# Performance work log

Measured on AMD Instinct MI355X. Metric: run time of the kernel, lower is better.

## Reference

```python
import jax, jax.numpy as jnp
import numpy as np

D_MODEL = 1024
N_HEADS = 16
D_K = D_MODEL // N_HEADS  # 64, also d_v
B, S = 8, 1024


def setup_inputs() -> dict:
    key = jax.random.key(0)
    ks = jax.random.split(key, 12)
    sc = 1.0 / np.sqrt(D_MODEL)
    inp = {
        "q": jax.random.normal(ks[0], (B, S, D_MODEL), jnp.float32),
        "k": jax.random.normal(ks[1], (B, S, D_MODEL), jnp.float32),
        "v": jax.random.normal(ks[2], (B, S, D_MODEL), jnp.float32),
        # per-head projection weights stacked over heads; torch Linear stores [out,in]
        "Wq": jax.random.normal(ks[3], (N_HEADS, D_K, D_MODEL), jnp.float32) * sc,
        "bq": jax.random.normal(ks[4], (N_HEADS, D_K), jnp.float32) * sc,
        "Wk": jax.random.normal(ks[5], (N_HEADS, D_K, D_MODEL), jnp.float32) * sc,
        "bk": jax.random.normal(ks[6], (N_HEADS, D_K), jnp.float32) * sc,
        "Wv": jax.random.normal(ks[7], (N_HEADS, D_K, D_MODEL), jnp.float32) * sc,
        "bv": jax.random.normal(ks[8], (N_HEADS, D_K), jnp.float32) * sc,
        "Wf": jax.random.normal(ks[9], (D_MODEL, D_MODEL), jnp.float32) * sc,
        "bf": jax.random.normal(ks[10], (D_MODEL,), jnp.float32) * sc,
    }
    return inp


def reference(q, k, v, Wq, bq, Wk, bk, Wv, bv, Wf, bf):
    temper = jnp.asarray(D_K ** 0.5, q.dtype)
    # per-head linear projections, all heads at once: [b,s,h,dk]
    qh = jnp.einsum('bsd,hkd->bhsk', q, Wq) + bq[None, :, None, :]
    kh = jnp.einsum('bsd,hkd->bhsk', k, Wk) + bk[None, :, None, :]
    vh = jnp.einsum('bsd,hkd->bhsk', v, Wv) + bv[None, :, None, :]
    # scaled dot-product scores [b,h,s,s]
    scores = jnp.einsum('bhik,bhjk->bhij', qh, kh) / temper
    # faithful scalar-equality mask: positions exactly equal to mask (=0) -> -inf
    scores = jnp.where(scores == 0.0, -jnp.inf, scores)
    attn = jax.nn.softmax(scores, axis=-1)
    out = jnp.einsum('bhij,bhjv->bhiv', attn, vh)  # [b,h,s,dv]
    # concat heads (head order matches torch.cat over ModuleList)
    out = out.transpose(0, 2, 1, 3).reshape(out.shape[0], out.shape[2], -1)  # [b,s,d_model]
    return out @ Wf.T + bf
```

## Files before the change

### kernel.cpp

```cpp
#include <hip/hip_runtime.h>
#include <hip/hip_bf16.h>


#define D_MODEL_ 1024
#define NH_ 16
#define DK_ 64
#define B_ 8
#define S_ 1024
#define M_ (B_ * S_)

typedef __hip_bfloat16 bf16;
typedef __attribute__((ext_vector_type(8))) short short8;
typedef __attribute__((ext_vector_type(4))) short short4_t;
typedef __attribute__((ext_vector_type(4))) float f32x4;

typedef const __attribute__((address_space(1))) unsigned int* gas_u32p;
typedef __attribute__((address_space(3))) unsigned int* las_u32p;

__device__ __forceinline__ short f2bs(float x) {
  bf16 h = __float2bfloat16(x);
  return *reinterpret_cast<short*>(&h);
}

__global__ __launch_bounds__(256)
void conv_f32_bf16(const float* __restrict__ in, bf16* __restrict__ out) {
  size_t i = ((size_t)blockIdx.x * 256 + threadIdx.x) * 8;
  f32x4 a = *(const f32x4*)(in + i);
  f32x4 b = *(const f32x4*)(in + i + 4);
  short8 s;
  s[0] = f2bs(a[0]); s[1] = f2bs(a[1]); s[2] = f2bs(a[2]); s[3] = f2bs(a[3]);
  s[4] = f2bs(b[0]); s[5] = f2bs(b[1]); s[6] = f2bs(b[2]); s[7] = f2bs(b[3]);
  *(short8*)((short*)out + i) = s;
}

__global__ __launch_bounds__(256)
void conv_w4(const float* __restrict__ w0, const float* __restrict__ w1,
             const float* __restrict__ w2, const float* __restrict__ w3,
             bf16* __restrict__ out) {
  const float* src = (blockIdx.z == 0) ? w0 : (blockIdx.z == 1) ? w1
                   : (blockIdx.z == 2) ? w2 : w3;
  size_t i = ((size_t)blockIdx.x * 256 + threadIdx.x) * 8;
  f32x4 a = *(const f32x4*)(src + i);
  f32x4 b = *(const f32x4*)(src + i + 4);
  short8 s;
  s[0] = f2bs(a[0]); s[1] = f2bs(a[1]); s[2] = f2bs(a[2]); s[3] = f2bs(a[3]);
  s[4] = f2bs(b[0]); s[5] = f2bs(b[1]); s[6] = f2bs(b[2]); s[7] = f2bs(b[3]);
  *(short8*)((short*)out + (size_t)blockIdx.z * 1024 * 1024 + i) = s;
}

__global__ __launch_bounds__(256)
void gemm_mfma(const void* __restrict__ A, const bf16* __restrict__ Wb,
               const float* __restrict__ bias, void* __restrict__ C,
               int aF32, int cMode, float cscale)
{
  __shared__ short As[2][2][128 * 32];
  __shared__ short Bs[2][2][128 * 32];
  const int tid = threadIdx.x;
  const int lane = tid & 63;
  const int w = tid >> 6;
  const int l15 = lane & 15, quad = lane >> 4;
  const int wm = (w >> 1) * 64, wn = (w & 1) * 64;
  const int m0 = blockIdx.x * 128, n0 = blockIdx.y * 128;

  const int srow = (lane >> 2);
  const int skc  = (lane & 3) * 8;

  f32x4 au[4], av[4];

  auto stageA = [&](int buf, int k0) {
    const bf16* Ab = (const bf16*)A;
#pragma unroll
    for (int sub = 0; sub < 2; ++sub)
#pragma unroll
      for (int p = 0; p < 2; ++p) {
        int r = 32 * w + 16 * p + srow;
        __builtin_amdgcn_global_load_lds(
            (gas_u32p)(const void*)(Ab + (size_t)(m0 + r) * 1024 + k0 + sub * 32 + skc),
            (las_u32p)(void*)((char*)&As[buf][sub][0] + w * 2048 + p * 1024), 16, 0, 0);
      }
  };
  auto stageB = [&](int buf, int k0) {
#pragma unroll
    for (int sub = 0; sub < 2; ++sub)
#pragma unroll
      for (int p = 0; p < 2; ++p) {
        int r = 32 * w + 16 * p + srow;
        __builtin_amdgcn_global_load_lds(
            (gas_u32p)(const void*)(Wb + (size_t)(n0 + r) * 1024 + k0 + sub * 32 + skc),
            (las_u32p)(void*)((char*)&Bs[buf][sub][0] + w * 2048 + p * 1024), 16, 0, 0);
      }
  };
  auto loadAf = [&](int k0) {
    const float* Af = (const float*)A;
#pragma unroll
    for (int p = 0; p < 4; ++p) {
      int c = p * 256 + tid;
      int r = c >> 3, kc = (c & 7) * 8;
      const float* g = Af + (size_t)(m0 + r) * 1024 + k0 + kc;
      au[p] = *(const f32x4*)g;
      av[p] = *(const f32x4*)(g + 4);
    }
  };
  auto writeAf = [&](int buf) {
#pragma unroll
    for (int p = 0; p < 4; ++p) {
      int c = p * 256 + tid;
      int r = c >> 3, kc = (c & 7) * 8;
      short8 s;
      s[0] = f2bs(au[p][0]); s[1] = f2bs(au[p][1]); s[2] = f2bs(au[p][2]); s[3] = f2bs(au[p][3]);
      s[4] = f2bs(av[p][0]); s[5] = f2bs(av[p][1]); s[6] = f2bs(av[p][2]); s[7] = f2bs(av[p][3]);
      *(short8*)&As[buf][kc >> 5][r * 32 + (kc & 31)] = s;
    }
  };

  f32x4 acc[4][4];
#pragma unroll
  for (int i = 0; i < 4; ++i)
#pragma unroll
    for (int j = 0; j < 4; ++j)
      acc[i][j] = (f32x4){0.f, 0.f, 0.f, 0.f};

  if (aF32) { loadAf(0); writeAf(0); }
  else       stageA(0, 0);
  stageB(0, 0);
  __syncthreads();

#pragma unroll 2
  for (int k0 = 0; k0 < 1024; k0 += 64) {
    const int cur = (k0 >> 6) & 1;
    const int nxt = cur ^ 1;
    const bool pf = (k0 + 64) < 1024;

    if (pf) {
      if (aF32) loadAf(k0 + 64);
      else      stageA(nxt, k0 + 64);
      stageB(nxt, k0 + 64);
    }

#pragma unroll
    for (int kk = 0; kk < 2; ++kk) {
      short8 af[4], bfv[4];
#pragma unroll
      for (int t = 0; t < 4; ++t) {
        af[t]  = *(short8*)&As[cur][kk][(wm + t * 16 + l15) * 32 + quad * 8];
        bfv[t] = *(short8*)&Bs[cur][kk][(wn + t * 16 + l15) * 32 + quad * 8];
      }
#pragma unroll
      for (int mt = 0; mt < 4; ++mt)
#pragma unroll
        for (int nt = 0; nt < 4; ++nt)
          acc[mt][nt] = __builtin_amdgcn_mfma_f32_16x16x32_bf16(af[mt], bfv[nt], acc[mt][nt], 0, 0, 0);
    }

    if (pf && aF32) writeAf(nxt);

    __syncthreads();
  }

  if (cMode == 2) {
    bf16* vt = (bf16*)C;
    const int bidx = m0 >> 10;
    const int sbase = (m0 & 1023) + wm;
#pragma unroll
    for (int nt = 0; nt < 4; ++nt) {
      int n = n0 + wn + nt * 16 + l15;
      float bv = bias[n];
#pragma unroll
      for (int mt = 0; mt < 4; ++mt) {
        int s = sbase + mt * 16 + quad * 4;
        short4_t pk;
#pragma unroll
        for (int r = 0; r < 4; ++r) pk[r] = f2bs((acc[mt][nt][r] + bv) * cscale);
        *(short4_t*)((short*)vt + ((size_t)bidx * 1024 + n) * 1024 + s) = pk;
      }
    }
  } else {
#pragma unroll
    for (int nt = 0; nt < 4; ++nt) {
      int col = n0 + wn + nt * 16 + l15;
      float bv = bias[col];
#pragma unroll
      for (int mt = 0; mt < 4; ++mt)
#pragma unroll
        for (int r = 0; r < 4; ++r) {
          int row = m0 + wm + mt * 16 + quad * 4 + r;
          float val = (acc[mt][nt][r] + bv) * cscale;
          if (cMode == 1) ((float*)C)[(size_t)row * 1024 + col] = val;
          else ((bf16*)C)[(size_t)row * 1024 + col] = __float2bfloat16(val);
        }
    }
  }
}

__global__ __launch_bounds__(256)
void attn_mfma(const bf16* __restrict__ QH, const bf16* __restrict__ KH,
               const bf16* __restrict__ VT, bf16* __restrict__ AO)
{
  __shared__ short Ks[2][64 * 32];
  __shared__ short Vs[2][64 * 32];
  __shared__ short Ps[4][16 * 72];
  const int tid = threadIdx.x;
  const int lane = tid & 63;
  const int w = tid >> 6;
  const int l15 = lane & 15, quad = lane >> 4;
  const int q0 = blockIdx.x * 64;
  const int h = blockIdx.y, b = blockIdx.z;
  const size_t base = ((size_t)b * S_) * D_MODEL_ + (size_t)h * DK_;
  const size_t vtb  = (((size_t)b * NH_ + h) * DK_) * (size_t)S_;
  const float NEG = -1e30f;
  short* myPs = Ps[w];

  const int srow = 16 * w + (lane >> 2);
  const int skc  = (lane & 3) * 8;

  short8 qa[2];
#pragma unroll
  for (int ks = 0; ks < 2; ++ks)
    qa[ks] = *(const short8*)((const short*)QH + base + (size_t)(q0 + w * 16 + l15) * D_MODEL_ + ks * 32 + quad * 8);

  float mi = NEG, li = 0.f;
  f32x4 oacc[4];
#pragma unroll
  for (int nt = 0; nt < 4; ++nt) oacc[nt] = (f32x4){0.f, 0.f, 0.f, 0.f};

  for (int j0 = 0; j0 < S_; j0 += 64) {
    __syncthreads();
#pragma unroll
    for (int sub = 0; sub < 2; ++sub) {
      __builtin_amdgcn_global_load_lds(
          (gas_u32p)(const void*)((const short*)KH + base + (size_t)(j0 + srow) * D_MODEL_ + sub * 32 + skc),
          (las_u32p)(void*)((char*)&Ks[sub][0] + w * 1024), 16, 0, 0);
      __builtin_amdgcn_global_load_lds(
          (gas_u32p)(const void*)((const short*)VT + vtb + (size_t)srow * S_ + j0 + sub * 32 + skc),
          (las_u32p)(void*)((char*)&Vs[sub][0] + w * 1024), 16, 0, 0);
    }
    __syncthreads();

    short8 kb[4][2], vb[4][2];
#pragma unroll
    for (int nt = 0; nt < 4; ++nt)
#pragma unroll
      for (int ks = 0; ks < 2; ++ks) {
        kb[nt][ks] = *(short8*)&Ks[ks][(nt * 16 + l15) * 32 + quad * 8];
        vb[nt][ks] = *(short8*)&Vs[ks][(nt * 16 + l15) * 32 + quad * 8];
      }

    f32x4 sacc[4];
#pragma unroll
    for (int nt = 0; nt < 4; ++nt) sacc[nt] = (f32x4){0.f, 0.f, 0.f, 0.f};
    __builtin_amdgcn_s_setprio(1);
#pragma unroll
    for (int nt = 0; nt < 4; ++nt)
#pragma unroll
      for (int ks = 0; ks < 2; ++ks)
        sacc[nt] = __builtin_amdgcn_mfma_f32_16x16x32_bf16(kb[nt][ks], qa[ks], sacc[nt], 0, 0, 0);
    __builtin_amdgcn_s_setprio(0);

    float p[4][4];
#pragma unroll
    for (int nt = 0; nt < 4; ++nt)
#pragma unroll
      for (int r = 0; r < 4; ++r) {
        float x = sacc[nt][r];
        if (x == 0.0f) x = NEG;
        p[nt][r] = x;
      }
    float mm[4];
#pragma unroll
    for (int nt = 0; nt < 4; ++nt)
      mm[nt] = fmaxf(fmaxf(p[nt][0], p[nt][1]), fmaxf(p[nt][2], p[nt][3]));
    float rm = fmaxf(fmaxf(mm[0], mm[1]), fmaxf(mm[2], mm[3]));
    rm = fmaxf(rm, __shfl_xor(rm, 16, 64));
    rm = fmaxf(rm, __shfl_xor(rm, 32, 64));

    const bool skip = __all(rm <= mi + 8.0f);
    const float nm = skip ? mi : fmaxf(mi, rm);

    float psum[4];
#pragma unroll
    for (int nt = 0; nt < 4; ++nt) {
      float e0 = __expf(p[nt][0] - nm), e1 = __expf(p[nt][1] - nm);
      float e2 = __expf(p[nt][2] - nm), e3 = __expf(p[nt][3] - nm);
      p[nt][0] = e0; p[nt][1] = e1; p[nt][2] = e2; p[nt][3] = e3;
      psum[nt] = (e0 + e1) + (e2 + e3);
    }
    float ps = (psum[0] + psum[1]) + (psum[2] + psum[3]);
    ps += __shfl_xor(ps, 16, 64);
    ps += __shfl_xor(ps, 32, 64);

    if (skip) {
      li += ps;
    } else {
      float alpha = __expf(mi - nm);
      li = li * alpha + ps;
      float ar[4];
#pragma unroll
      for (int r = 0; r < 4; ++r) ar[r] = __shfl(alpha, quad * 4 + r, 64);
#pragma unroll
      for (int nt = 0; nt < 4; ++nt)
#pragma unroll
        for (int r = 0; r < 4; ++r) oacc[nt][r] *= ar[r];
    }
    mi = nm;

#pragma unroll
    for (int nt = 0; nt < 4; ++nt) {
      short4_t pk;
#pragma unroll
      for (int r = 0; r < 4; ++r) pk[r] = f2bs(p[nt][r]);
      *(short4_t*)&myPs[l15 * 72 + nt * 16 + quad * 4] = pk;
    }

    __threadfence_block();

    short8 pa[2];
#pragma unroll
    for (int ks = 0; ks < 2; ++ks)
      pa[ks] = *(short8*)&myPs[l15 * 72 + ks * 32 + quad * 8];
    __builtin_amdgcn_s_setprio(1);
#pragma unroll
    for (int nt = 0; nt < 4; ++nt)
#pragma unroll
      for (int ks = 0; ks < 2; ++ks)
        oacc[nt] = __builtin_amdgcn_mfma_f32_16x16x32_bf16(pa[ks], vb[nt][ks], oacc[nt], 0, 0, 0);
    __builtin_amdgcn_s_setprio(0);
  }

  float lr[4];
#pragma unroll
  for (int r = 0; r < 4; ++r) lr[r] = __shfl(li, quad * 4 + r, 64);
#pragma unroll
  for (int r = 0; r < 4; ++r) {
    float inv = (lr[r] > 0.f) ? 1.0f / lr[r] : 0.f;
    int q = q0 + w * 16 + quad * 4 + r;
#pragma unroll
    for (int nt = 0; nt < 4; ++nt)
      AO[base + (size_t)q * D_MODEL_ + nt * 16 + l15] = __float2bfloat16(oacc[nt][r] * inv);
  }
}

extern "C" void kernel_launch(void* const* d_in, const int* in_sizes, int n_in,
                              void* d_out, int out_size, void* d_ws, size_t ws_size,
                              hipStream_t stream) {
  (void)in_sizes; (void)n_in; (void)out_size; (void)ws_size;
  const float* q  = (const float*)d_in[0];
  const float* k  = (const float*)d_in[1];
  const float* v  = (const float*)d_in[2];
  const float* Wq = (const float*)d_in[3];
  const float* bq = (const float*)d_in[4];
  const float* Wk = (const float*)d_in[5];
  const float* bk = (const float*)d_in[6];
  const float* Wv = (const float*)d_in[7];
  const float* bv = (const float*)d_in[8];
  const float* Wf = (const float*)d_in[9];
  const float* bF = (const float*)d_in[10];

  const size_t MB = (size_t)1024 * 1024;
  char* ws = (char*)d_ws;
  bf16* wb4 = (bf16*)(ws);
  bf16* wqb = wb4;
  bf16* wkb = (bf16*)(ws + 2 * MB);
  bf16* wvb = (bf16*)(ws + 4 * MB);
  bf16* wfb = (bf16*)(ws + 6 * MB);
  bf16* inb = (bf16*)(ws + 8 * MB);
  bf16* vt  = (bf16*)(ws + 16 * MB);
  bf16* qh  = (bf16*)d_out;
  bf16* kh  = (bf16*)((char*)d_out + 16 * MB);

  dim3 blk(256);
  dim3 igrid(4096);
  dim3 ggrid(M_ / 128, D_MODEL_ / 128);

  conv_w4<<<dim3(512, 1, 4), blk, 0, stream>>>(Wq, Wk, Wv, Wf, wb4);

  conv_f32_bf16<<<igrid, blk, 0, stream>>>(q, inb);
  gemm_mfma<<<ggrid, blk, 0, stream>>>(inb, wqb, bq, qh, 0, 0, 0.125f);
  conv_f32_bf16<<<igrid, blk, 0, stream>>>(k, inb);
  gemm_mfma<<<ggrid, blk, 0, stream>>>(inb, wkb, bk, kh, 0, 0, 1.0f);
  gemm_mfma<<<ggrid, blk, 0, stream>>>(v, wvb, bv, vt, 1, 2, 1.0f);

  attn_mfma<<<dim3(S_ / 64, NH_, B_), blk, 0, stream>>>(qh, kh, vt, qh);

  hipMemcpyAsync(inb, d_out, 16 * MB, hipMemcpyDeviceToDevice, stream);
  gemm_mfma<<<ggrid, blk, 0, stream>>>(inb, wfb, bF, d_out, 0, 1, 1.0f);
}
```

Measured before the change: 361.3 us.

## Fuse QKV projections into one launch, swizzle LDS, and drop conversion passes

Replaces the separate fp32-to-bf16 conversion kernels and three projection GEMM launches with one gemm_proj launch (grid z=3) that converts fp32 A in registers on the fly. It adds an XOR swizzle to the LDS layouts in both the GEMM and attention kernels to reduce bank conflicts. The GEMM drops double buffering in favour of a single LDS buffer with register prefetch, which halves shared memory. The final GEMM uses 128x64 tiles for more blocks, and when the workspace is large enough the attention output goes to a separate buffer so the device-to-device copy is skipped. The risks are less load/compute overlap in the single-buffered GEMM and more register pressure from the on-the-fly conversion.

```diff
diff --git a/kernel.cpp b/kernel.cpp
--- a/kernel.cpp
+++ b/kernel.cpp
@@ -20,17 +20,6 @@
 __device__ __forceinline__ short f2bs(float x) {
   bf16 h = __float2bfloat16(x);
   return *reinterpret_cast<short*>(&h);
-}
-
-__global__ __launch_bounds__(256)
-void conv_f32_bf16(const float* __restrict__ in, bf16* __restrict__ out) {
-  size_t i = ((size_t)blockIdx.x * 256 + threadIdx.x) * 8;
-  f32x4 a = *(const f32x4*)(in + i);
-  f32x4 b = *(const f32x4*)(in + i + 4);
-  short8 s;
-  s[0] = f2bs(a[0]); s[1] = f2bs(a[1]); s[2] = f2bs(a[2]); s[3] = f2bs(a[3]);
-  s[4] = f2bs(b[0]); s[5] = f2bs(b[1]); s[6] = f2bs(b[2]); s[7] = f2bs(b[3]);
-  *(short8*)((short*)out + i) = s;
 }
 
 __global__ __launch_bounds__(256)
@@ -48,48 +37,25 @@
   *(short8*)((short*)out + (size_t)blockIdx.z * 1024 * 1024 + i) = s;
 }
 
-__global__ __launch_bounds__(256)
-void gemm_mfma(const void* __restrict__ A, const bf16* __restrict__ Wb,
-               const float* __restrict__ bias, void* __restrict__ C,
-               int aF32, int cMode, float cscale)
+template<int BN, int AF32>
+__device__ __forceinline__ void gemm_body(const void* __restrict__ A,
+                                          const bf16* __restrict__ Wb,
+                                          const float* __restrict__ bias,
+                                          void* __restrict__ C,
+                                          int cMode, float cscale, int m0, int n0)
 {
-  __shared__ short As[2][2][128 * 32];
-  __shared__ short Bs[2][2][128 * 32];
+  __shared__ short As[2][128 * 32];
+  __shared__ short Bs[2][BN * 32];
   const int tid = threadIdx.x;
   const int lane = tid & 63;
   const int w = tid >> 6;
   const int l15 = lane & 15, quad = lane >> 4;
-  const int wm = (w >> 1) * 64, wn = (w & 1) * 64;
-  const int m0 = blockIdx.x * 128, n0 = blockIdx.y * 128;
-
-  const int srow = (lane >> 2);
-  const int skc  = (lane & 3) * 8;
+  const int wm = (w >> 1) * 64, wn = (w & 1) * (BN / 2);
+  const int srow = lane >> 2;
+  const int sslot = ((lane & 3) ^ ((lane >> 3) & 3)) * 8;
+  const int rsl = (quad ^ ((l15 >> 1) & 3)) * 8;
 
   f32x4 au[4], av[4];
-
-  auto stageA = [&](int buf, int k0) {
-    const bf16* Ab = (const bf16*)A;
-#pragma unroll
-    for (int sub = 0; sub < 2; ++sub)
-#pragma unroll
-      for (int p = 0; p < 2; ++p) {
-        int r = 32 * w + 16 * p + srow;
-        __builtin_amdgcn_global_load_lds(
-            (gas_u32p)(const void*)(Ab + (size_t)(m0 + r) * 1024 + k0 + sub * 32 + skc),
-            (las_u32p)(void*)((char*)&As[buf][sub][0] + w * 2048 + p * 1024), 16, 0, 0);
-      }
-  };
-  auto stageB = [&](int buf, int k0) {
-#pragma unroll
-    for (int sub = 0; sub < 2; ++sub)
-#pragma unroll
-      for (int p = 0; p < 2; ++p) {
-        int r = 32 * w + 16 * p + srow;
-        __builtin_amdgcn_global_load_lds(
-            (gas_u32p)(const void*)(Wb + (size_t)(n0 + r) * 1024 + k0 + sub * 32 + skc),
-            (las_u32p)(void*)((char*)&Bs[buf][sub][0] + w * 2048 + p * 1024), 16, 0, 0);
-      }
-  };
   auto loadAf = [&](int k0) {
     const float* Af = (const float*)A;
 #pragma unroll
@@ -101,60 +67,72 @@
       av[p] = *(const f32x4*)(g + 4);
     }
   };
-  auto writeAf = [&](int buf) {
+  auto writeAf = [&]() {
 #pragma unroll
     for (int p = 0; p < 4; ++p) {
       int c = p * 256 + tid;
       int r = c >> 3, kc = (c & 7) * 8;
-      short8 s;
-      s[0] = f2bs(au[p][0]); s[1] = f2bs(au[p][1]); s[2] = f2bs(au[p][2]); s[3] = f2bs(au[p][3]);
-      s[4] = f2bs(av[p][0]); s[5] = f2bs(av[p][1]); s[6] = f2bs(av[p][2]); s[7] = f2bs(av[p][3]);
-      *(short8*)&As[buf][kc >> 5][r * 32 + (kc & 31)] = s;
+      int s = (c & 3) ^ ((r >> 1) & 3);
+      short8 sv;
+      sv[0] = f2bs(au[p][0]); sv[1] = f2bs(au[p][1]); sv[2] = f2bs(au[p][2]); sv[3] = f2bs(au[p][3]);
+      sv[4] = f2bs(av[p][0]); sv[5] = f2bs(av[p][1]); sv[6] = f2bs(av[p][2]); sv[7] = f2bs(av[p][3]);
+      *(short8*)&As[kc >> 5][r * 32 + s * 8] = sv;
     }
   };
 
-  f32x4 acc[4][4];
+  f32x4 acc[4][BN / 32];
 #pragma unroll
   for (int i = 0; i < 4; ++i)
 #pragma unroll
-    for (int j = 0; j < 4; ++j)
+    for (int j = 0; j < BN / 32; ++j)
       acc[i][j] = (f32x4){0.f, 0.f, 0.f, 0.f};
 
-  if (aF32) { loadAf(0); writeAf(0); }
-  else       stageA(0, 0);
-  stageB(0, 0);
-  __syncthreads();
-
-#pragma unroll 2
+  if (AF32) loadAf(0);
+
   for (int k0 = 0; k0 < 1024; k0 += 64) {
-    const int cur = (k0 >> 6) & 1;
-    const int nxt = cur ^ 1;
-    const bool pf = (k0 + 64) < 1024;
-
-    if (pf) {
-      if (aF32) loadAf(k0 + 64);
-      else      stageA(nxt, k0 + 64);
-      stageB(nxt, k0 + 64);
-    }
+    __syncthreads();
+    if (AF32) {
+      writeAf();
+    } else {
+      const bf16* Ab = (const bf16*)A;
+#pragma unroll
+      for (int sub = 0; sub < 2; ++sub)
+#pragma unroll
+        for (int p = 0; p < 2; ++p) {
+          int r = 32 * w + 16 * p + srow;
+          __builtin_amdgcn_global_load_lds(
+              (gas_u32p)(const void*)(Ab + (size_t)(m0 + r) * 1024 + k0 + sub * 32 + sslot),
+              (las_u32p)(void*)((char*)&As[sub][0] + w * 2048 + p * 1024), 16, 0, 0);
+        }
+    }
+#pragma unroll
+    for (int sub = 0; sub < 2; ++sub)
+#pragma unroll
+      for (int p = 0; p < BN / 64; ++p) {
+        int r = (BN / 4) * w + 16 * p + srow;
+        __builtin_amdgcn_global_load_lds(
+            (gas_u32p)(const void*)(Wb + (size_t)(n0 + r) * 1024 + k0 + sub * 32 + sslot),
+            (las_u32p)(void*)((char*)&Bs[sub][0] + w * (BN / 4) * 64 + p * 1024), 16, 0, 0);
+      }
+    __syncthreads();
+
+    if (AF32 && k0 + 64 < 1024) loadAf(k0 + 64);
 
 #pragma unroll
     for (int kk = 0; kk < 2; ++kk) {
-      short8 af[4], bfv[4];
-#pragma unroll
-      for (int t = 0; t < 4; ++t) {
-        af[t]  = *(short8*)&As[cur][kk][(wm + t * 16 + l15) * 32 + quad * 8];
-        bfv[t] = *(short8*)&Bs[cur][kk][(wn + t * 16 + l15) * 32 + quad * 8];
-      }
+      short8 af[4], bfv[BN / 32];
+#pragma unroll
+      for (int t = 0; t < 4; ++t)
+        af[t]  = *(short8*)&As[kk][(wm + t * 16 + l15) * 32 + rsl];
+#pragma unroll
+      for (int t = 0; t < BN / 32; ++t)
+        bfv[t] = *(short8*)&Bs[kk][(wn + t * 16 + l15) * 32 + rsl];
 #pragma unroll
       for (int mt = 0; mt < 4; ++mt)
 #pragma unroll
-        for (int nt = 0; nt < 4; ++nt)
+        for (int nt = 0; nt < BN / 32; ++nt)
           acc[mt][nt] = __builtin_amdgcn_mfma_f32_16x16x32_bf16(af[mt], bfv[nt], acc[mt][nt], 0, 0, 0);
     }
-
-    if (pf && aF32) writeAf(nxt);
-
-    __syncthreads();
   }
 
   if (cMode == 2) {
@@ -162,7 +140,7 @@
     const int bidx = m0 >> 10;
     const int sbase = (m0 & 1023) + wm;
 #pragma unroll
-    for (int nt = 0; nt < 4; ++nt) {
+    for (int nt = 0; nt < BN / 32; ++nt) {
       int n = n0 + wn + nt * 16 + l15;
       float bv = bias[n];
 #pragma unroll
@@ -176,7 +154,7 @@
     }
   } else {
 #pragma unroll
-    for (int nt = 0; nt < 4; ++nt) {
+    for (int nt = 0; nt < BN / 32; ++nt) {
       int col = n0 + wn + nt * 16 + l15;
       float bv = bias[col];
 #pragma unroll
@@ -190,6 +168,31 @@
         }
     }
   }
+}
+
+__global__ __launch_bounds__(256)
+void gemm_proj(const float* __restrict__ q, const float* __restrict__ k,
+               const float* __restrict__ v, const bf16* __restrict__ wq,
+               const bf16* __restrict__ wk, const bf16* __restrict__ wv,
+               const float* __restrict__ bq, const float* __restrict__ bk,
+               const float* __restrict__ bv, void* __restrict__ cq,
+               void* __restrict__ ck, void* __restrict__ cv)
+{
+  const int z = blockIdx.z;
+  const float* A = (z == 0) ? q : (z == 1) ? k : v;
+  const bf16* W  = (z == 0) ? wq : (z == 1) ? wk : wv;
+  const float* bb = (z == 0) ? bq : (z == 1) ? bk : bv;
+  void* C = (z == 0) ? cq : (z == 1) ? ck : cv;
+  int cMode = (z == 2) ? 2 : 0;
+  float cscale = (z == 0) ? 0.125f : 1.0f;
+  gemm_body<128, 1>(A, W, bb, C, cMode, cscale, blockIdx.x * 128, blockIdx.y * 128);
+}
+
+__global__ __launch_bounds__(256)
+void gemm_final(const bf16* __restrict__ A, const bf16* __restrict__ W,
+                const float* __restrict__ bias, void* __restrict__ C)
+{
+  gemm_body<64, 0>(A, W, bias, C, 1, 1.0f, blockIdx.x * 128, blockIdx.y * 64);
 }
 
 __global__ __launch_bounds__(256)
@@ -211,7 +214,8 @@
   short* myPs = Ps[w];
 
   const int srow = 16 * w + (lane >> 2);
-  const int skc  = (lane & 3) * 8;
+  const int sslot = ((lane & 3) ^ ((lane >> 3) & 3)) * 8;
+  const int rsl = (quad ^ ((l15 >> 1) & 3)) * 8;
 
   short8 qa[2];
 #pragma unroll
@@ -228,10 +232,10 @@
 #pragma unroll
     for (int sub = 0; sub < 2; ++sub) {
       __builtin_amdgcn_global_load_lds(
-          (gas_u32p)(const void*)((const short*)KH + base + (size_t)(j0 + srow) * D_MODEL_ + sub * 32 + skc),
+          (gas_u32p)(const void*)((const short*)KH + base + (size_t)(j0 + srow) * D_MODEL_ + sub * 32 + sslot),
           (las_u32p)(void*)((char*)&Ks[sub][0] + w * 1024), 16, 0, 0);
       __builtin_amdgcn_global_load_lds(
-          (gas_u32p)(const void*)((const short*)VT + vtb + (size_t)srow * S_ + j0 + sub * 32 + skc),
+          (gas_u32p)(const void*)((const short*)VT + vtb + (size_t)srow * S_ + j0 + sub * 32 + sslot),
           (las_u32p)(void*)((char*)&Vs[sub][0] + w * 1024), 16, 0, 0);
     }
     __syncthreads();
@@ -241,8 +245,8 @@
     for (int nt = 0; nt < 4; ++nt)
 #pragma unroll
       for (int ks = 0; ks < 2; ++ks) {
-        kb[nt][ks] = *(short8*)&Ks[ks][(nt * 16 + l15) * 32 + quad * 8];
-        vb[nt][ks] = *(short8*)&Vs[ks][(nt * 16 + l15) * 32 + quad * 8];
+        kb[nt][ks] = *(short8*)&Ks[ks][(nt * 16 + l15) * 32 + rsl];
+        vb[nt][ks] = *(short8*)&Vs[ks][(nt * 16 + l15) * 32 + rsl];
       }
 
     f32x4 sacc[4];
@@ -342,7 +346,7 @@
 extern "C" void kernel_launch(void* const* d_in, const int* in_sizes, int n_in,
                               void* d_out, int out_size, void* d_ws, size_t ws_size,
                               hipStream_t stream) {
-  (void)in_sizes; (void)n_in; (void)out_size; (void)ws_size;
+  (void)in_sizes; (void)n_in; (void)out_size;
   const float* q  = (const float*)d_in[0];
   const float* k  = (const float*)d_in[1];
   const float* v  = (const float*)d_in[2];
@@ -357,30 +361,29 @@
 
   const size_t MB = (size_t)1024 * 1024;
   char* ws = (char*)d_ws;
-  bf16* wb4 = (bf16*)(ws);
-  bf16* wqb = wb4;
+  bf16* wqb = (bf16*)(ws);
   bf16* wkb = (bf16*)(ws + 2 * MB);
   bf16* wvb = (bf16*)(ws + 4 * MB);
   bf16* wfb = (bf16*)(ws + 6 * MB);
-  bf16* inb = (bf16*)(ws + 8 * MB);
-  bf16* vt  = (bf16*)(ws + 16 * MB);
+  bf16* vt  = (bf16*)(ws + 8 * MB);
   bf16* qh  = (bf16*)d_out;
   bf16* kh  = (bf16*)((char*)d_out + 16 * MB);
 
+  const bool bigws = ws_size >= (size_t)40 * MB;
+  bf16* aob = bigws ? (bf16*)(ws + 24 * MB) : qh;
+  bf16* fin = bigws ? aob : (bf16*)(ws + 8 * MB);
+
   dim3 blk(256);
-  dim3 igrid(4096);
-  dim3 ggrid(M_ / 128, D_MODEL_ / 128);
-
-  conv_w4<<<dim3(512, 1, 4), blk, 0, stream>>>(Wq, Wk, Wv, Wf, wb4);
-
-  conv_f32_bf16<<<igrid, blk, 0, stream>>>(q, inb);
-  gemm_mfma<<<ggrid, blk, 0, stream>>>(inb, wqb, bq, qh, 0, 0, 0.125f);
-  conv_f32_bf16<<<igrid, blk, 0, stream>>>(k, inb);
-  gemm_mfma<<<ggrid, blk, 0, stream>>>(inb, wkb, bk, kh, 0, 0, 1.0f);
-  gemm_mfma<<<ggrid, blk, 0, stream>>>(v, wvb, bv, vt, 1, 2, 1.0f);
-
-  attn_mfma<<<dim3(S_ / 64, NH_, B_), blk, 0, stream>>>(qh, kh, vt, qh);
-
-  hipMemcpyAsync(inb, d_out, 16 * MB, hipMemcpyDeviceToDevice, stream);
-  gemm_mfma<<<ggrid, blk, 0, stream>>>(inb, wfb, bF, d_out, 0, 1, 1.0f);
-}
+
+  conv_w4<<<dim3(512, 1, 4), blk, 0, stream>>>(Wq, Wk, Wv, Wf, wqb);
+
+  gemm_proj<<<dim3(M_ / 128, D_MODEL_ / 128, 3), blk, 0, stream>>>(
+      q, k, v, wqb, wkb, wvb, bq, bk, bv, qh, kh, vt);
+
+  attn_mfma<<<dim3(S_ / 64, NH_, B_), blk, 0, stream>>>(qh, kh, vt, aob);
+
+  if (!bigws)
+    hipMemcpyAsync(ws + 8 * MB, d_out, 16 * MB, hipMemcpyDeviceToDevice, stream);
+
+  gemm_final<<<dim3(M_ / 128, D_MODEL_ / 64), blk, 0, stream>>>(fin, wfb, bF, d_out);
+}
```

Result: faster. 330.3 us (-8.6%).
